# Performance work log

Measured on AMD Instinct MI355X. Metric: run time of the kernel, lower is better.

Reference implementation:

```python
import jax, jax.numpy as jnp
import numpy as np

B, S, H = 1, 4096, 2048
NH, NKV, HD = 16, 4, 128
EPS = 1e-5
THETA = 10000.0


def rms_norm(x, w, eps=EPS):
    var = jnp.mean(jnp.square(x), axis=-1, keepdims=True)
    return x * jax.lax.rsqrt(var + eps) * w


def rotate_half(x):
    x1, x2 = jnp.split(x, 2, axis=-1)
    return jnp.concatenate([-x2, x1], axis=-1)


def rope_cos_sin(seq_len, head_dim, dtype):
    inv_freq = 1.0 / (THETA ** (jnp.arange(0, head_dim, 2, dtype=jnp.float32) / head_dim))
    t = jnp.arange(seq_len, dtype=jnp.float32)
    freqs = jnp.outer(t, inv_freq)                      # [S, HD/2]
    emb = jnp.concatenate([freqs, freqs], axis=-1)      # [S, HD]
    return jnp.cos(emb).astype(dtype), jnp.sin(emb).astype(dtype)


def setup_inputs() -> dict:
    key = jax.random.key(0)
    ks = jax.random.split(key, 5)
    return {
        "hidden_states": jax.random.normal(ks[0], (B, S, H), jnp.float32),
        "wq": jax.random.normal(ks[1], (NH * HD, H), jnp.float32) * 0.02,
        "wk": jax.random.normal(ks[2], (NKV * HD, H), jnp.float32) * 0.02,
        "wv": jax.random.normal(ks[3], (NKV * HD, H), jnp.float32) * 0.02,
        "wo": jax.random.normal(ks[4], (H, NH * HD), jnp.float32) * 0.02,
        "q_norm_w": jnp.ones((NH * HD,), jnp.float32),
        "k_norm_w": jnp.ones((NKV * HD,), jnp.float32),
    }


def reference(hidden_states, wq, wk, wv, wo, q_norm_w, k_norm_w):
    b, s, _ = hidden_states.shape
    n_rep = NH // NKV

    # projections + QK RMSNorm (applied over the full flattened head dim, pre-split)
    q = rms_norm(hidden_states @ wq.T, q_norm_w)        # [B,S,NH*HD]
    k = rms_norm(hidden_states @ wk.T, k_norm_w)        # [B,S,NKV*HD]
    v = hidden_states @ wv.T                            # [B,S,NKV*HD]

    # split heads -> [B, heads, S, HD]
    q = q.reshape(b, s, NH, HD).transpose(0, 2, 1, 3)
    k = k.reshape(b, s, NKV, HD).transpose(0, 2, 1, 3)
    v = v.reshape(b, s, NKV, HD).transpose(0, 2, 1, 3)

    # RoPE (position_ids = arange(s))
    cos, sin = rope_cos_sin(s, HD, q.dtype)             # [S, HD]
    cos = cos[None, None]                               # [1,1,S,HD]
    sin = sin[None, None]
    q = q * cos + rotate_half(q) * sin
    k = k * cos + rotate_half(k) * sin

    # GQA attention without physical KV repeat: q -> [B, NKV, n_rep, S, HD]
    qg = q.reshape(b, NKV, n_rep, s, HD)
    scale = 1.0 / np.sqrt(HD)
    scores = jnp.einsum('bgrqd,bgkd->bgrqk', qg, k) * scale   # [B,NKV,rep,S,S]

    causal = jnp.tril(jnp.ones((s, s), bool))
    scores = jnp.where(causal, scores, jnp.finfo(scores.dtype).min)

    probs = jax.nn.softmax(scores.astype(jnp.float32), axis=-1).astype(q.dtype)
    out = jnp.einsum('bgrqk,bgkd->bgrqd', probs, v)           # [B,NKV,rep,S,HD]

    # merge heads -> [B,S,NH*HD], output projection
    out = out.reshape(b, NH, s, HD).transpose(0, 2, 1, 3).reshape(b, s, NH * HD)
    return out @ wo.T
```

## Files before the change

kernel.cpp:

```cpp
#include <hip/hip_runtime.h>
#include <math.h>

#define S_LEN 4096
#define HIDDEN 2048
#define N_HEADS 16
#define N_KV 4
#define HEAD_DIM 128
#define QDIM 2048
#define KDIM 512
#define QKVD 3072
#define QSCALE 0.1275174486f

typedef __bf16 bf16x8 __attribute__((ext_vector_type(8)));
typedef float f32x4 __attribute__((ext_vector_type(4)));
typedef float f32x16 __attribute__((ext_vector_type(16)));

__device__ __forceinline__ unsigned short f2bf(float x) {
  union { float f; unsigned u; } v; v.f = x;
  unsigned r = v.u + 0x7fffu + ((v.u >> 16) & 1u);
  return (unsigned short)(r >> 16);
}
__device__ __forceinline__ float bf2f(unsigned short u) {
  union { unsigned u; float f; } v; v.u = ((unsigned)u) << 16;
  return v.f;
}

__device__ __forceinline__ float wave_sum(float x) {
#pragma unroll
  for (int w = 32; w >= 1; w >>= 1) x += __shfl_xor(x, w);
  return x;
}

__global__ void k_cvt(const float* __restrict__ s, unsigned short* __restrict__ d, int n4) {
  int i = blockIdx.x * blockDim.x + threadIdx.x;
  if (i >= n4) return;
  float4 v = reinterpret_cast<const float4*>(s)[i];
  ushort4 o;
  o.x = f2bf(v.x); o.y = f2bf(v.y); o.z = f2bf(v.z); o.w = f2bf(v.w);
  reinterpret_cast<ushort4*>(d)[i] = o;
}

__global__ void k_rope_tab(float* __restrict__ cosT, float* __restrict__ sinT) {
  int idx = blockIdx.x * blockDim.x + threadIdx.x;
  int s = idx >> 6, d = idx & 63;
  float inv = powf(10000.0f, -(float)(2 * d) * (1.0f / 128.0f));
  float f = (float)s * inv;
  cosT[idx] = cosf(f);
  sinT[idx] = sinf(f);
}

#define BM 128
#define BN 128
#define BK 32

__global__ __launch_bounds__(256) void k_gemm_bt(
    const unsigned short* __restrict__ A, const unsigned short* __restrict__ B,
    float* __restrict__ C, int M, int N, int K) {
  __shared__ unsigned short lds[2][BM * BK + BN * BK];
  const int tid = threadIdx.x;
  const int wave = tid >> 6, lane = tid & 63;
  const int brow = blockIdx.y * BM, bcol = blockIdx.x * BN;
  const int wr = wave >> 1, wc = wave & 1;
  const unsigned short* Ab = A + (size_t)brow * K;
  const unsigned short* Bb = B + (size_t)bcol * K;
  const int r0 = tid >> 2;
  const int c0 = (tid & 3) * 8;

  f32x4 acc[4][4] = {};

#pragma unroll
  for (int c = 0; c < 2; ++c) {
    __builtin_amdgcn_global_load_lds(
        (const __attribute__((address_space(1))) void*)(Ab + (size_t)(c * 64 + r0) * K + c0),
        (__attribute__((address_space(3))) void*)(&lds[0][(c * 64 + r0) * BK + c0]), 16, 0, 0);
    __builtin_amdgcn_global_load_lds(
        (const __attribute__((address_space(1))) void*)(Bb + (size_t)(c * 64 + r0) * K + c0),
        (__attribute__((address_space(3))) void*)(&lds[0][BM * BK + (c * 64 + r0) * BK + c0]), 16, 0, 0);
  }

  const int KT = K / BK;
  const int arow = wr * 64 + (lane & 15);
  const int brow2 = wc * 64 + (lane & 15);
  const int koff = (lane >> 4) * 8;

  for (int kt = 0; kt < KT; ++kt) {
    if (kt + 1 < KT) {
      const int k0 = (kt + 1) * BK;
      const int buf = (kt + 1) & 1;
#pragma unroll
      for (int c = 0; c < 2; ++c) {
        __builtin_amdgcn_global_load_lds(
            (const __attribute__((address_space(1))) void*)(Ab + (size_t)(c * 64 + r0) * K + k0 + c0),
            (__attribute__((address_space(3))) void*)(&lds[buf][(c * 64 + r0) * BK + c0]), 16, 0, 0);
        __builtin_amdgcn_global_load_lds(
            (const __attribute__((address_space(1))) void*)(Bb + (size_t)(c * 64 + r0) * K + k0 + c0),
            (__attribute__((address_space(3))) void*)(&lds[buf][BM * BK + (c * 64 + r0) * BK + c0]), 16, 0, 0);
      }
    }
    __syncthreads();
    const unsigned short* la = &lds[kt & 1][0];
    const unsigned short* lb = &lds[kt & 1][BM * BK];
    bf16x8 a[4], b[4];
#pragma unroll
    for (int m = 0; m < 4; ++m)
      a[m] = *reinterpret_cast<const bf16x8*>(la + (arow + m * 16) * BK + koff);
#pragma unroll
    for (int n = 0; n < 4; ++n)
      b[n] = *reinterpret_cast<const bf16x8*>(lb + (brow2 + n * 16) * BK + koff);
#pragma unroll
    for (int m = 0; m < 4; ++m)
#pragma unroll
      for (int n = 0; n < 4; ++n)
        acc[m][n] = __builtin_amdgcn_mfma_f32_16x16x32_bf16(a[m], b[n], acc[m][n], 0, 0, 0);
    __syncthreads();
  }

  const int crow = brow + wr * 64 + (lane >> 4) * 4;
  const int ccol = bcol + wc * 64 + (lane & 15);
#pragma unroll
  for (int m = 0; m < 4; ++m)
#pragma unroll
    for (int n = 0; n < 4; ++n)
#pragma unroll
      for (int i = 0; i < 4; ++i)
        C[(size_t)(crow + m * 16 + i) * N + ccol + n * 16] = acc[m][n][i];
}

__global__ __launch_bounds__(256) void k_norm_rope(
    const float* __restrict__ QKV, const float* __restrict__ qw, const float* __restrict__ kw,
    const float* __restrict__ cosT, const float* __restrict__ sinT,
    unsigned short* __restrict__ Q, unsigned short* __restrict__ Kd, unsigned short* __restrict__ Vt) {
  const int s = blockIdx.x;
  const int tid = threadIdx.x;
  const int lane = tid & 63, wave = tid >> 6;
  const float* row = QKV + (size_t)s * QKVD;
  __shared__ float sm[QDIM];
  __shared__ float red[4];

  float qv[8];
  *reinterpret_cast<float4*>(&qv[0]) = reinterpret_cast<const float4*>(row)[tid * 2];
  *reinterpret_cast<float4*>(&qv[4]) = reinterpret_cast<const float4*>(row)[tid * 2 + 1];
  float ss = 0;
#pragma unroll
  for (int j = 0; j < 8; ++j) ss += qv[j] * qv[j];
  ss = wave_sum(ss);
  if (lane == 0) red[wave] = ss;
  __syncthreads();
  float tot = red[0] + red[1] + red[2] + red[3];
  float qs = rsqrtf(tot * (1.0f / QDIM) + 1e-5f) * QSCALE;
#pragma unroll
  for (int j = 0; j < 8; ++j) sm[tid * 8 + j] = qv[j] * qs * qw[tid * 8 + j];
  __syncthreads();
  {
    const int d0 = tid * 8;
    const int h = d0 >> 7;
    const int dh = d0 & 127;
    const int dc = dh & 63;
    const bool lo = dh < 64;
    const float sgn = lo ? -1.0f : 1.0f;
    const int po = lo ? 64 : -64;
    union { unsigned short b[8]; uint4 u; } pk;
#pragma unroll
    for (int j = 0; j < 8; ++j) {
      float c = cosT[s * 64 + dc + j];
      float sn = sinT[s * 64 + dc + j];
      float o = sm[d0 + j] * c + sgn * sm[d0 + po + j] * sn;
      pk.b[j] = f2bf(o);
    }
    *reinterpret_cast<uint4*>(Q + ((size_t)h * S_LEN + s) * HEAD_DIM + dh) = pk.u;
  }
  __syncthreads();

  float2 kvp = *reinterpret_cast<const float2*>(row + QDIM + tid * 2);
  ss = kvp.x * kvp.x + kvp.y * kvp.y;
  ss = wave_sum(ss);
  if (lane == 0) red[wave] = ss;
  __syncthreads();
  tot = red[0] + red[1] + red[2] + red[3];
  float ks = rsqrtf(tot * (1.0f / KDIM) + 1e-5f);
  sm[tid * 2] = kvp.x * ks * kw[tid * 2];
  sm[tid * 2 + 1] = kvp.y * ks * kw[tid * 2 + 1];
  __syncthreads();
  {
    const int d0 = tid * 2;
    const int g = d0 >> 7;
    const int dh = d0 & 127;
    const int dc = dh & 63;
    const bool lo = dh < 64;
    const float sgn = lo ? -1.0f : 1.0f;
    const int po = lo ? 64 : -64;
    union { unsigned short b[2]; unsigned u; } pk;
#pragma unroll
    for (int j = 0; j < 2; ++j) {
      float c = cosT[s * 64 + dc + j];
      float sn = sinT[s * 64 + dc + j];
      float o = sm[d0 + j] * c + sgn * sm[d0 + po + j] * sn;
      pk.b[j] = f2bf(o);
    }
    *reinterpret_cast<unsigned*>(Kd + ((size_t)g * S_LEN + s) * HEAD_DIM + dh) = pk.u;
  }

  {
    float2 vv = *reinterpret_cast<const float2*>(row + QDIM + KDIM + tid * 2);
    int dv = tid * 2;
    int g = dv >> 7, d = dv & 127;
    Vt[(size_t)(g * HEAD_DIM + d) * S_LEN + s] = f2bf(vv.x);
    Vt[(size_t)(g * HEAD_DIM + d + 1) * S_LEN + s] = f2bf(vv.y);
  }
}

__global__ __launch_bounds__(256, 3) void k_attn(
    const unsigned short* __restrict__ Q, const unsigned short* __restrict__ K,
    const unsigned short* __restrict__ Vt,
    unsigned short* __restrict__ Op0, unsigned short* __restrict__ Op1,
    float* __restrict__ Mp, float* __restrict__ Lp) {
  const int bid = blockIdx.x;
  const int qt = 127 - (bid >> 3);
  const int sub = bid & 7;
  const int g = sub >> 1, half = sub & 1;
  const int NT = qt + 1, ntlo = (NT + 1) >> 1;
  const int t0 = half ? ntlo : 0, t1 = half ? NT : ntlo;

  const int tid = threadIdx.x;
  const int w = tid >> 6, lane = tid & 63;
  const int l31 = lane & 31, g2 = lane >> 5;
  const int h = g * 4 + w;
  const int qpos = qt * 32;

  unsigned short* __restrict__ Op = half ? Op1 : Op0;
  float* __restrict__ Mh = Mp + half * (16 * 4096);
  float* __restrict__ Lh = Lp + half * (16 * 4096);

  if (t0 >= t1) {
    if (g2 == 0) {
      Mh[h * 4096 + qpos + l31] = -1e30f;
      Lh[h * 4096 + qpos + l31] = 0.f;
    }
    return;
  }

  __shared__ char lds[2][16384];

  const char* Kgb = (const char*)(K + (size_t)g * S_LEN * HEAD_DIM);
  const char* Vgb = (const char*)(Vt + (size_t)g * HEAD_DIM * S_LEN);

  const bool isK = (w < 2);
  const int wj = isK ? w : (w - 2);

#define STAGE(BUFP, KV0)                                                                  \
  {                                                                                       \
    char* dstb = (BUFP);                                                                  \
    _Pragma("unroll")                                                                     \
    for (int j = 0; j < 4; ++j) {                                                         \
      if (isK) {                                                                          \
        const int r = (wj * 4 + j) * 4 + (lane >> 4);                                     \
        const char* src = Kgb + (size_t)((KV0) + r) * 256 +                               \
                          (((lane & 15) * 16) ^ ((r & 15) << 4));                         \
        __builtin_amdgcn_global_load_lds(                                                 \
            (const __attribute__((address_space(1))) void*)src,                           \
            (__attribute__((address_space(3))) void*)(dstb + (wj * 4 + j) * 1024),        \
            16, 0, 0);                                                                    \
      } else {                                                                            \
        const int r = (wj * 4 + j) * 8 + (lane >> 3);                                     \
        const int cu = ((lane & 7) * 16) ^ ((r & 7) << 4);                                \
        const int dd = 2 * r + (cu >> 6);                                                 \
        const char* src = Vgb + (size_t)dd * 8192 + (size_t)(KV0) * 2 + (cu & 63);        \
        __builtin_amdgcn_global_load_lds(                                                 \
            (const __attribute__((address_space(1))) void*)src,                           \
            (__attribute__((address_space(3))) void*)(dstb + 8192 + (wj * 4 + j) * 1024), \
            16, 0, 0);                                                                    \
      }                                                                                   \
    }                                                                                     \
  }

  STAGE(lds[0], t0 * 32)

  bf16x8 qf[8];
#pragma unroll
  for (int dc2 = 0; dc2 < 8; ++dc2)
    qf[dc2] = *reinterpret_cast<const bf16x8*>(
        Q + ((size_t)h * S_LEN + qpos + l31) * HEAD_DIM + dc2 * 16 + g2 * 8);

  f32x16 o[4] = {};
  float m = -1e30f, l = 0.f;

  for (int t = t0; t < t1; ++t) {
    char* buf = lds[(t - t0) & 1];
    __syncthreads();
    if (t + 1 < t1) STAGE(lds[(t - t0 + 1) & 1], (t + 1) * 32)
    const char* Kl = buf;
    const char* Vl = buf + 8192;
    const int kv0 = t * 32;

    f32x16 sc = {};
    __builtin_amdgcn_s_setprio(1);
#pragma unroll
    for (int dc2 = 0; dc2 < 8; ++dc2) {
      bf16x8 kf = *reinterpret_cast<const bf16x8*>(
          Kl + l31 * 256 + ((dc2 * 32 + g2 * 16) ^ ((l31 & 15) << 4)));
      sc = __builtin_amdgcn_mfma_f32_32x32x16_bf16(kf, qf[dc2], sc, 0, 0, 0);
    }
    __builtin_amdgcn_s_setprio(0);
    if (t == qt) {
#pragma unroll
      for (int reg = 0; reg < 16; ++reg) {
        int kv = kv0 + (reg & 3) + 8 * (reg >> 2) + 4 * g2;
        if (kv > qpos + l31) sc[reg] = -1e30f;
      }
    }
    float pm = sc[0];
#pragma unroll
    for (int i = 1; i < 16; ++i) pm = fmaxf(pm, sc[i]);
    pm = fmaxf(pm, __shfl_xor(pm, 32));
    if (!__all(pm <= m + 8.f)) {
      float mn = fmaxf(m, pm);
      float fac = __builtin_amdgcn_exp2f(m - mn);
#pragma unroll
      for (int dc = 0; dc < 4; ++dc) o[dc] *= fac;
      l *= fac;
      m = mn;
    }
    union { __bf16 b[16]; unsigned u[8]; } P;
    float rs = 0.f;
#pragma unroll
    for (int i = 0; i < 16; ++i) {
      float p = __builtin_amdgcn_exp2f(sc[i] - m);
      rs += p;
      P.b[i] = (__bf16)p;
    }
    rs += __shfl_xor(rs, 32);
    l += rs;
    uint4 pf[2];
#pragma unroll
    for (int c16 = 0; c16 < 2; ++c16) {
      unsigned A0 = P.u[c16 * 4], A1 = P.u[c16 * 4 + 1];
      unsigned A2 = P.u[c16 * 4 + 2], A3 = P.u[c16 * 4 + 3];
      unsigned A0x = __shfl_xor(A0, 32), A1x = __shfl_xor(A1, 32);
      unsigned A2x = __shfl_xor(A2, 32), A3x = __shfl_xor(A3, 32);
      pf[c16].x = g2 ? A2x : A0;
      pf[c16].y = g2 ? A3x : A1;
      pf[c16].z = g2 ? A2 : A0x;
      pf[c16].w = g2 ? A3 : A1x;
    }
    __builtin_amdgcn_s_setprio(1);
#pragma unroll
    for (int c16 = 0; c16 < 2; ++c16) {
      union { uint4 u; bf16x8 v; } cv;
      cv.u = pf[c16];
#pragma unroll
      for (int dc = 0; dc < 4; ++dc) {
        const int r = dc * 16 + (l31 >> 1);
        const int cu = (l31 & 1) * 64 + c16 * 32 + g2 * 16;
        bf16x8 vf = *reinterpret_cast<const bf16x8*>(Vl + r * 128 + (cu ^ ((r & 7) << 4)));
        o[dc] = __builtin_amdgcn_mfma_f32_32x32x16_bf16(vf, cv.v, o[dc], 0, 0, 0);
      }
    }
    __builtin_amdgcn_s_setprio(0);
  }

  if (g2 == 0) {
    Mh[h * 4096 + qpos + l31] = m;
    Lh[h * 4096 + qpos + l31] = l;
  }
#pragma unroll
  for (int dc = 0; dc < 4; ++dc)
#pragma unroll
    for (int reg = 0; reg < 16; ++reg) {
      int d = dc * 32 + (reg & 3) + 8 * (reg >> 2) + 4 * g2;
      Op[(((size_t)(h * 128 + d)) << 12) + qpos + l31] = f2bf(o[dc][reg]);
    }
#undef STAGE
}

__global__ __launch_bounds__(256) void k_combine(
    const unsigned short* __restrict__ Op0, const unsigned short* __restrict__ Op1,
    const float* __restrict__ Mp, const float* __restrict__ Lp,
    unsigned short* __restrict__ AO) {
  const int idx = blockIdx.x * 256 + threadIdx.x;
  const int h = idx >> 12, q = idx & 4095;
  const float m0 = Mp[h * 4096 + q], m1 = Mp[16 * 4096 + h * 4096 + q];
  const float l0 = Lp[h * 4096 + q], l1 = Lp[16 * 4096 + h * 4096 + q];
  const float mm = fmaxf(m0, m1);
  const float w0 = __builtin_amdgcn_exp2f(m0 - mm);
  const float w1 = __builtin_amdgcn_exp2f(m1 - mm);
  const float denom = w0 * l0 + w1 * l1;
  const float c0 = w0 / denom, c1 = w1 / denom;
  const bool has1 = (l1 > 0.f);
  const size_t bq = ((size_t)h * 128) << 12;
#pragma unroll
  for (int halfd = 0; halfd < 2; ++halfd) {
    float acc[64];
#pragma unroll
    for (int i = 0; i < 64; ++i) {
      const size_t off = bq + (((size_t)(halfd * 64 + i)) << 12) + q;
      float v = c0 * bf2f(Op0[off]);
      if (has1) v += c1 * bf2f(Op1[off]);
      acc[i] = v;
    }
#pragma unroll
    for (int dc = 0; dc < 8; ++dc) {
      union { unsigned short s[8]; uint4 u; } pk;
#pragma unroll
      for (int j = 0; j < 8; ++j) pk.s[j] = f2bf(acc[dc * 8 + j]);
      *reinterpret_cast<uint4*>(AO + (size_t)q * QDIM + h * 128 + halfd * 64 + dc * 8) = pk.u;
    }
  }
}

extern "C" void kernel_launch(void* const* d_in, const int* in_sizes, int n_in,
                              void* d_out, int out_size, void* d_ws, size_t ws_size,
                              hipStream_t stream) {
  const float* hs = (const float*)d_in[0];
  const float* wq = (const float*)d_in[1];
  const float* wk = (const float*)d_in[2];
  const float* wv = (const float*)d_in[3];
  const float* wo = (const float*)d_in[4];
  const float* qnw = (const float*)d_in[5];
  const float* knw = (const float*)d_in[6];
  float* out = (float*)d_out;

  char* base = (char*)d_ws;
  unsigned short* Xb = (unsigned short*)base;
  unsigned short* Qb = Xb;
  unsigned short* Wqkv = (unsigned short*)(base + 16777216);
  unsigned short* Kb = Wqkv;
  unsigned short* Vtb = (unsigned short*)(base + 20971520);
  float* Mp = (float*)(base + 25165824);
  float* Lp = (float*)(base + 25690112);
  unsigned short* Wob = (unsigned short*)(base + 29360128);
  float* QKV = (float*)(base + 37748736);
  unsigned short* AOb = (unsigned short*)QKV;
  unsigned short* Op0 = (unsigned short*)(base + 54525952);
  unsigned short* Op1 = (unsigned short*)(base + 71303168);
  float* cosT = (float*)(base + 88080384);
  float* sinT = (float*)(base + 89128960);

  int n;
  n = S_LEN * HIDDEN / 4; k_cvt<<<(n + 255) / 256, 256, 0, stream>>>(hs, Xb, n);
  n = QDIM * HIDDEN / 4;  k_cvt<<<(n + 255) / 256, 256, 0, stream>>>(wq, Wqkv, n);
  n = KDIM * HIDDEN / 4;  k_cvt<<<(n + 255) / 256, 256, 0, stream>>>(wk, Wqkv + (size_t)QDIM * HIDDEN, n);
  n = KDIM * HIDDEN / 4;  k_cvt<<<(n + 255) / 256, 256, 0, stream>>>(wv, Wqkv + (size_t)(QDIM + KDIM) * HIDDEN, n);
  n = HIDDEN * QDIM / 4;  k_cvt<<<(n + 255) / 256, 256, 0, stream>>>(wo, Wob, n);
  k_rope_tab<<<(S_LEN * 64) / 256, 256, 0, stream>>>(cosT, sinT);

  k_gemm_bt<<<dim3(QKVD / BN, S_LEN / BM), 256, 0, stream>>>(Xb, Wqkv, QKV, S_LEN, QKVD, HIDDEN);
  k_norm_rope<<<S_LEN, 256, 0, stream>>>(QKV, qnw, knw, cosT, sinT, Qb, Kb, Vtb);
  k_attn<<<1024, 256, 0, stream>>>(Qb, Kb, Vtb, Op0, Op1, Mp, Lp);
  k_combine<<<256, 256, 0, stream>>>(Op0, Op1, Mp, Lp, AOb);
  k_gemm_bt<<<dim3(QDIM / BN, S_LEN / BM), 256, 0, stream>>>(AOb, Wob, out, S_LEN, QDIM, HIDDEN);
}
```

Baseline: 343.0 us.

## Rewrite GEMM with BK=64 swizzled LDS pipeline and bf16 QKV output

Replaces the GEMM kernel with a version that uses 64-wide K tiles, an XOR-swizzled LDS layout to avoid bank conflicts, explicit vmcnt/lgkmcnt waits with one barrier per step, prefetch two stages ahead, and setprio around the MFMA block. The QKV projection now writes bf16 instead of fp32, halving intermediate traffic, and norm_rope reads bf16. This rounds QKV to bf16 before RMSNorm, which costs some precision, and the 64KB LDS with two blocks per CU may limit occupancy.

```diff
diff --git a/kernel.cpp b/kernel.cpp
--- a/kernel.cpp
+++ b/kernel.cpp
@@ -49,97 +49,139 @@
   sinT[idx] = sinf(f);
 }
 
-#define BM 128
-#define BN 128
-#define BK 32
-
-__global__ __launch_bounds__(256) void k_gemm_bt(
+#define GKT (HIDDEN / 64)
+
+template <int BF16OUT>
+__global__ __launch_bounds__(256, 2) void k_gemm(
     const unsigned short* __restrict__ A, const unsigned short* __restrict__ B,
-    float* __restrict__ C, int M, int N, int K) {
-  __shared__ unsigned short lds[2][BM * BK + BN * BK];
+    void* __restrict__ Cv, int N) {
+  __shared__ char ldsb[65536];
   const int tid = threadIdx.x;
-  const int wave = tid >> 6, lane = tid & 63;
-  const int brow = blockIdx.y * BM, bcol = blockIdx.x * BN;
-  const int wr = wave >> 1, wc = wave & 1;
-  const unsigned short* Ab = A + (size_t)brow * K;
-  const unsigned short* Bb = B + (size_t)bcol * K;
-  const int r0 = tid >> 2;
-  const int c0 = (tid & 3) * 8;
+  const int w = tid >> 6, lane = tid & 63;
+  const int l15 = lane & 15, g16 = lane >> 4;
+  const int wm = w >> 1, wn = w & 1;
+  const int brow = blockIdx.y * 128, bcol = blockIdx.x * 128;
+  const char* Abp = (const char*)(A + (size_t)brow * HIDDEN);
+  const char* Bbp = (const char*)(B + (size_t)bcol * HIDDEN);
+
+#define GSTAGE(bi, kt)                                                              \
+  {                                                                                 \
+    _Pragma("unroll")                                                               \
+    for (int j = 0; j < 4; ++j) {                                                   \
+      const int slot = w * 256 + j * 64 + lane;                                     \
+      const int r = slot >> 3;                                                      \
+      const int cb = (slot & 7) * 16;                                               \
+      const char* srcA = Abp + (size_t)r * (2 * HIDDEN) + (kt) * 128 +              \
+                         (cb ^ ((r & 7) << 4));                                     \
+      __builtin_amdgcn_global_load_lds(                                             \
+          (const __attribute__((address_space(1))) void*)srcA,                      \
+          (__attribute__((address_space(3))) void*)(ldsb + (bi)*16384 + slot * 16), \
+          16, 0, 0);                                                                \
+      const char* srcB = Bbp + (size_t)r * (2 * HIDDEN) + (kt) * 128 +              \
+                         (cb ^ ((r & 7) << 4));                                     \
+      __builtin_amdgcn_global_load_lds(                                             \
+          (const __attribute__((address_space(1))) void*)srcB,                      \
+          (__attribute__((address_space(3))) void*)(ldsb + 32768 + (bi)*16384 +     \
+                                                    slot * 16),                     \
+          16, 0, 0);                                                                \
+    }                                                                               \
+  }
 
   f32x4 acc[4][4] = {};
 
-#pragma unroll
-  for (int c = 0; c < 2; ++c) {
-    __builtin_amdgcn_global_load_lds(
-        (const __attribute__((address_space(1))) void*)(Ab + (size_t)(c * 64 + r0) * K + c0),
-        (__attribute__((address_space(3))) void*)(&lds[0][(c * 64 + r0) * BK + c0]), 16, 0, 0);
-    __builtin_amdgcn_global_load_lds(
-        (const __attribute__((address_space(1))) void*)(Bb + (size_t)(c * 64 + r0) * K + c0),
-        (__attribute__((address_space(3))) void*)(&lds[0][BM * BK + (c * 64 + r0) * BK + c0]), 16, 0, 0);
-  }
-
-  const int KT = K / BK;
-  const int arow = wr * 64 + (lane & 15);
-  const int brow2 = wc * 64 + (lane & 15);
-  const int koff = (lane >> 4) * 8;
-
-  for (int kt = 0; kt < KT; ++kt) {
-    if (kt + 1 < KT) {
-      const int k0 = (kt + 1) * BK;
-      const int buf = (kt + 1) & 1;
-#pragma unroll
-      for (int c = 0; c < 2; ++c) {
-        __builtin_amdgcn_global_load_lds(
-            (const __attribute__((address_space(1))) void*)(Ab + (size_t)(c * 64 + r0) * K + k0 + c0),
-            (__attribute__((address_space(3))) void*)(&lds[buf][(c * 64 + r0) * BK + c0]), 16, 0, 0);
-        __builtin_amdgcn_global_load_lds(
-            (const __attribute__((address_space(1))) void*)(Bb + (size_t)(c * 64 + r0) * K + k0 + c0),
-            (__attribute__((address_space(3))) void*)(&lds[buf][BM * BK + (c * 64 + r0) * BK + c0]), 16, 0, 0);
+  GSTAGE(0, 0)
+  GSTAGE(1, 1)
+  asm volatile("s_waitcnt vmcnt(8)" ::: "memory");
+  __builtin_amdgcn_sched_barrier(0);
+  __builtin_amdgcn_s_barrier();
+  __builtin_amdgcn_sched_barrier(0);
+
+  for (int kt = 0; kt < GKT; ++kt) {
+    const char* Al = ldsb + (kt & 1) * 16384;
+    const char* Bl = ldsb + 32768 + (kt & 1) * 16384;
+    bf16x8 a[4][2], b[4][2];
+#pragma unroll
+    for (int fm = 0; fm < 4; ++fm) {
+      const int r = wm * 64 + fm * 16 + l15;
+#pragma unroll
+      for (int kh = 0; kh < 2; ++kh)
+        a[fm][kh] = *reinterpret_cast<const bf16x8*>(
+            Al + r * 128 + ((kh * 64 + g16 * 16) ^ ((r & 7) << 4)));
+    }
+#pragma unroll
+    for (int fn = 0; fn < 4; ++fn) {
+      const int r = wn * 64 + fn * 16 + l15;
+#pragma unroll
+      for (int kh = 0; kh < 2; ++kh)
+        b[fn][kh] = *reinterpret_cast<const bf16x8*>(
+            Bl + r * 128 + ((kh * 64 + g16 * 16) ^ ((r & 7) << 4)));
+    }
+    asm volatile("s_waitcnt lgkmcnt(0)" ::: "memory");
+    __builtin_amdgcn_sched_barrier(0);
+    __builtin_amdgcn_s_barrier();
+    __builtin_amdgcn_sched_barrier(0);
+    if (kt + 2 < GKT) GSTAGE(kt & 1, kt + 2)
+    __builtin_amdgcn_s_setprio(1);
+#pragma unroll
+    for (int kh = 0; kh < 2; ++kh)
+#pragma unroll
+      for (int fm = 0; fm < 4; ++fm)
+#pragma unroll
+        for (int fn = 0; fn < 4; ++fn)
+          acc[fm][fn] =
+              __builtin_amdgcn_mfma_f32_16x16x32_bf16(a[fm][kh], b[fn][kh], acc[fm][fn], 0, 0, 0);
+    __builtin_amdgcn_s_setprio(0);
+    if (kt + 1 < GKT) {
+      if (kt + 2 < GKT) {
+        asm volatile("s_waitcnt vmcnt(8)" ::: "memory");
+      } else {
+        asm volatile("s_waitcnt vmcnt(0)" ::: "memory");
       }
-    }
-    __syncthreads();
-    const unsigned short* la = &lds[kt & 1][0];
-    const unsigned short* lb = &lds[kt & 1][BM * BK];
-    bf16x8 a[4], b[4];
-#pragma unroll
-    for (int m = 0; m < 4; ++m)
-      a[m] = *reinterpret_cast<const bf16x8*>(la + (arow + m * 16) * BK + koff);
-#pragma unroll
-    for (int n = 0; n < 4; ++n)
-      b[n] = *reinterpret_cast<const bf16x8*>(lb + (brow2 + n * 16) * BK + koff);
-#pragma unroll
-    for (int m = 0; m < 4; ++m)
-#pragma unroll
-      for (int n = 0; n < 4; ++n)
-        acc[m][n] = __builtin_amdgcn_mfma_f32_16x16x32_bf16(a[m], b[n], acc[m][n], 0, 0, 0);
-    __syncthreads();
-  }
-
-  const int crow = brow + wr * 64 + (lane >> 4) * 4;
-  const int ccol = bcol + wc * 64 + (lane & 15);
-#pragma unroll
-  for (int m = 0; m < 4; ++m)
-#pragma unroll
-    for (int n = 0; n < 4; ++n)
-#pragma unroll
-      for (int i = 0; i < 4; ++i)
-        C[(size_t)(crow + m * 16 + i) * N + ccol + n * 16] = acc[m][n][i];
+      __builtin_amdgcn_sched_barrier(0);
+      __builtin_amdgcn_s_barrier();
+      __builtin_amdgcn_sched_barrier(0);
+    }
+  }
+
+  const int crow = brow + wm * 64 + g16 * 4;
+  const int ccol = bcol + wn * 64 + l15;
+#pragma unroll
+  for (int fm = 0; fm < 4; ++fm)
+#pragma unroll
+    for (int fn = 0; fn < 4; ++fn)
+#pragma unroll
+      for (int i = 0; i < 4; ++i) {
+        const size_t off = (size_t)(crow + fm * 16 + i) * N + ccol + fn * 16;
+        if (BF16OUT)
+          ((unsigned short*)Cv)[off] = f2bf(acc[fm][fn][i]);
+        else
+          ((float*)Cv)[off] = acc[fm][fn][i];
+      }
+#undef GSTAGE
 }
 
 __global__ __launch_bounds__(256) void k_norm_rope(
-    const float* __restrict__ QKV, const float* __restrict__ qw, const float* __restrict__ kw,
-    const float* __restrict__ cosT, const float* __restrict__ sinT,
-    unsigned short* __restrict__ Q, unsigned short* __restrict__ Kd, unsigned short* __restrict__ Vt) {
+    const unsigned short* __restrict__ QKV, const float* __restrict__ qw,
+    const float* __restrict__ kw, const float* __restrict__ cosT,
+    const float* __restrict__ sinT, unsigned short* __restrict__ Q,
+    unsigned short* __restrict__ Kd, unsigned short* __restrict__ Vt) {
   const int s = blockIdx.x;
   const int tid = threadIdx.x;
   const int lane = tid & 63, wave = tid >> 6;
-  const float* row = QKV + (size_t)s * QKVD;
+  const unsigned short* row = QKV + (size_t)s * QKVD;
   __shared__ float sm[QDIM];
   __shared__ float red[4];
 
   float qv[8];
-  *reinterpret_cast<float4*>(&qv[0]) = reinterpret_cast<const float4*>(row)[tid * 2];
-  *reinterpret_cast<float4*>(&qv[4]) = reinterpret_cast<const float4*>(row)[tid * 2 + 1];
+  {
+    uint4 r = *reinterpret_cast<const uint4*>(row + tid * 8);
+    unsigned u[4] = {r.x, r.y, r.z, r.w};
+#pragma unroll
+    for (int j = 0; j < 4; ++j) {
+      qv[2 * j] = bf2f((unsigned short)(u[j] & 0xffff));
+      qv[2 * j + 1] = bf2f((unsigned short)(u[j] >> 16));
+    }
+  }
   float ss = 0;
 #pragma unroll
   for (int j = 0; j < 8; ++j) ss += qv[j] * qv[j];
@@ -171,15 +213,20 @@
   }
   __syncthreads();
 
-  float2 kvp = *reinterpret_cast<const float2*>(row + QDIM + tid * 2);
-  ss = kvp.x * kvp.x + kvp.y * kvp.y;
+  float kx, ky;
+  {
+    unsigned kr = *reinterpret_cast<const unsigned*>(row + QDIM + tid * 2);
+    kx = bf2f((unsigned short)(kr & 0xffff));
+    ky = bf2f((unsigned short)(kr >> 16));
+  }
+  ss = kx * kx + ky * ky;
   ss = wave_sum(ss);
   if (lane == 0) red[wave] = ss;
   __syncthreads();
   tot = red[0] + red[1] + red[2] + red[3];
   float ks = rsqrtf(tot * (1.0f / KDIM) + 1e-5f);
-  sm[tid * 2] = kvp.x * ks * kw[tid * 2];
-  sm[tid * 2 + 1] = kvp.y * ks * kw[tid * 2 + 1];
+  sm[tid * 2] = kx * ks * kw[tid * 2];
+  sm[tid * 2 + 1] = ky * ks * kw[tid * 2 + 1];
   __syncthreads();
   {
     const int d0 = tid * 2;
@@ -201,11 +248,11 @@
   }
 
   {
-    float2 vv = *reinterpret_cast<const float2*>(row + QDIM + KDIM + tid * 2);
+    unsigned vr = *reinterpret_cast<const unsigned*>(row + QDIM + KDIM + tid * 2);
     int dv = tid * 2;
     int g = dv >> 7, d = dv & 127;
-    Vt[(size_t)(g * HEAD_DIM + d) * S_LEN + s] = f2bf(vv.x);
-    Vt[(size_t)(g * HEAD_DIM + d + 1) * S_LEN + s] = f2bf(vv.y);
+    Vt[(size_t)(g * HEAD_DIM + d) * S_LEN + s] = (unsigned short)(vr & 0xffff);
+    Vt[(size_t)(g * HEAD_DIM + d + 1) * S_LEN + s] = (unsigned short)(vr >> 16);
   }
 }
 
@@ -428,8 +475,8 @@
   float* Mp = (float*)(base + 25165824);
   float* Lp = (float*)(base + 25690112);
   unsigned short* Wob = (unsigned short*)(base + 29360128);
-  float* QKV = (float*)(base + 37748736);
-  unsigned short* AOb = (unsigned short*)QKV;
+  unsigned short* QKVb = (unsigned short*)(base + 37748736);
+  unsigned short* AOb = QKVb;
   unsigned short* Op0 = (unsigned short*)(base + 54525952);
   unsigned short* Op1 = (unsigned short*)(base + 71303168);
   float* cosT = (float*)(base + 88080384);
@@ -443,9 +490,9 @@
   n = HIDDEN * QDIM / 4;  k_cvt<<<(n + 255) / 256, 256, 0, stream>>>(wo, Wob, n);
   k_rope_tab<<<(S_LEN * 64) / 256, 256, 0, stream>>>(cosT, sinT);
 
-  k_gemm_bt<<<dim3(QKVD / BN, S_LEN / BM), 256, 0, stream>>>(Xb, Wqkv, QKV, S_LEN, QKVD, HIDDEN);
-  k_norm_rope<<<S_LEN, 256, 0, stream>>>(QKV, qnw, knw, cosT, sinT, Qb, Kb, Vtb);
+  k_gemm<1><<<dim3(QKVD / 128, S_LEN / 128), 256, 0, stream>>>(Xb, Wqkv, (void*)QKVb, QKVD);
+  k_norm_rope<<<S_LEN, 256, 0, stream>>>(QKVb, qnw, knw, cosT, sinT, Qb, Kb, Vtb);
   k_attn<<<1024, 256, 0, stream>>>(Qb, Kb, Vtb, Op0, Op1, Mp, Lp);
   k_combine<<<256, 256, 0, stream>>>(Op0, Op1, Mp, Lp, AOb);
-  k_gemm_bt<<<dim3(QDIM / BN, S_LEN / BM), 256, 0, stream>>>(AOb, Wob, out, S_LEN, QDIM, HIDDEN);
-}
+  k_gemm<0><<<dim3(QDIM / 128, S_LEN / 128), 256, 0, stream>>>(AOb, Wob, (void*)out, QDIM);
+}
```

New measurement: 314.1 us. 8.4% less time.
